# Performance work log

Measured on AMD Instinct MI355X. Metric: run time of the kernel, lower is better.

Reference implementation:

```python
import jax, jax.numpy as jnp
import numpy as np

GROUPS = 8
EPS = 1e-5


def setup_inputs() -> dict:
    key = jax.random.key(0)
    ks = jax.random.split(key, 3)
    b, c, h, w = 8, 256, 64, 64
    return {
        "x": jax.random.normal(ks[0], (b, c, h, w), dtype=jnp.float32),
        "norm_w": jnp.ones((c,), jnp.float32),
        "norm_b": jnp.zeros((c,), jnp.float32),
        "qkv_w": jax.random.normal(ks[1], (3 * c, c), dtype=jnp.float32) * (1.0 / np.sqrt(c)),
        "qkv_b": jnp.zeros((3 * c,), jnp.float32),
        "proj_w": jax.random.normal(ks[2], (c, c), dtype=jnp.float32) * (1.0 / np.sqrt(c)),
        "proj_b": jnp.zeros((c,), jnp.float32),
    }


def _group_norm(x, w, b):
    B, C, H, W = x.shape
    xg = x.reshape(B, GROUPS, C // GROUPS, H, W)
    mean = xg.mean(axis=(2, 3, 4), keepdims=True)
    var = xg.var(axis=(2, 3, 4), keepdims=True)
    xn = ((xg - mean) * jax.lax.rsqrt(var + EPS)).reshape(B, C, H, W)
    return xn * w[None, :, None, None] + b[None, :, None, None]


def reference(x, norm_w, norm_b, qkv_w, qkv_b, proj_w, proj_b):
    B, C, H, W = x.shape
    xn = _group_norm(x, norm_w, norm_b)
    # 1x1 conv == per-pixel matmul: [B,3C,H,W]
    qkv = jnp.einsum('bchw,oc->bohw', xn, qkv_w) + qkv_b[None, :, None, None]
    q, k, v = jnp.split(qkv, 3, axis=1)  # each [B,C,H,W]
    hw = H * W
    q = q.reshape(B, C, hw).transpose(0, 2, 1)  # [B,hw,C]
    k = k.reshape(B, C, hw)                     # [B,C,hw]
    v = v.reshape(B, C, hw).transpose(0, 2, 1)  # [B,hw,C]
    scores = jnp.einsum('bnc,bcm->bnm', q, k) / jnp.sqrt(jnp.asarray(C, x.dtype))
    attn = jax.nn.softmax(scores, axis=-1)      # [B,hw,hw]
    out = jnp.einsum('bnm,bmc->bnc', attn, v)   # [B,hw,C]
    out = out.transpose(0, 2, 1).reshape(B, C, H, W)
    out = jnp.einsum('bchw,oc->bohw', out, proj_w) + proj_b[None, :, None, None]
    return x + out
```

## Files before the change

kernel.cpp:

```cpp
#include <hip/hip_runtime.h>
#include <stdint.h>

#define BATCH 8
#define CH 256
#define HW 4096
#define OC 768

typedef __bf16 bf16;
typedef __attribute__((ext_vector_type(8))) __bf16 bf16x8;
typedef __attribute__((ext_vector_type(4))) __bf16 bf16x4;
typedef __attribute__((ext_vector_type(4))) float f32x4;
typedef __attribute__((ext_vector_type(4))) int i32x4;
typedef __attribute__((ext_vector_type(8))) int i32x8;
typedef long fp8x8;

#define MFMA16(a, b, c) __builtin_amdgcn_mfma_f32_16x16x32_bf16(a, b, c, 0, 0, 0)
#define MFMA8(a, b, c) __builtin_amdgcn_mfma_f32_16x16x32_fp8_fp8(a, b, c, 0, 0, 0)
#define MFMA_MX(a, b, c) __builtin_amdgcn_mfma_scale_f32_16x16x128_f8f6f4( \
    a, b, c, 0, 0, 0, 0x7F7F7F7F, 0, 0x7F7F7F7F)
#define LOG2E 1.44269504088896f

static __device__ __forceinline__ void gl2lds16(const void* g, void* l) {
  __builtin_amdgcn_global_load_lds((const __attribute__((address_space(1))) void*)g,
                                   (__attribute__((address_space(3))) void*)l, 16, 0, 0);
}

static __device__ __forceinline__ int pack4fp8(float a, float b, float c, float d) {
  int t = __builtin_amdgcn_cvt_pk_fp8_f32(a, b, 0, false);
  return __builtin_amdgcn_cvt_pk_fp8_f32(c, d, t, true);
}

__global__ __launch_bounds__(256) void trans_stats(const float* __restrict__ x,
    bf16* __restrict__ xt, float* __restrict__ partial) {
  __shared__ float tile[64][65];
  __shared__ float red[16];
  int b = blockIdx.z, ct = blockIdx.y, pt = blockIdx.x;
  int p0 = pt * 64, c0 = ct * 64;
  int tid = threadIdx.x;
  const float* xb = x + (size_t)b * CH * HW;
  float s[2] = {0.f, 0.f}, s2[2] = {0.f, 0.f};
#pragma unroll
  for (int i = 0; i < 4; i++) {
    int idx = i * 256 + tid;
    int c = idx >> 4, p4 = (idx & 15) * 4;
    float4 v = *(const float4*)(xb + (size_t)(c0 + c) * HW + p0 + p4);
    tile[c][p4] = v.x; tile[c][p4 + 1] = v.y; tile[c][p4 + 2] = v.z; tile[c][p4 + 3] = v.w;
    int g = i >> 1;
    s[g] += v.x + v.y + v.z + v.w;
    s2[g] += v.x * v.x + v.y * v.y + v.z * v.z + v.w * v.w;
  }
  for (int off = 32; off; off >>= 1) {
    s[0] += __shfl_down(s[0], off); s2[0] += __shfl_down(s2[0], off);
    s[1] += __shfl_down(s[1], off); s2[1] += __shfl_down(s2[1], off);
  }
  int wv = tid >> 6;
  if ((tid & 63) == 0) {
    red[wv * 4 + 0] = s[0]; red[wv * 4 + 1] = s2[0];
    red[wv * 4 + 2] = s[1]; red[wv * 4 + 3] = s2[1];
  }
  __syncthreads();
  if (tid < 2) {
    float ts = 0.f, ts2 = 0.f;
#pragma unroll
    for (int k = 0; k < 4; k++) { ts += red[k * 4 + tid * 2]; ts2 += red[k * 4 + tid * 2 + 1]; }
    float* pp = partial + ((size_t)(b * 8 + ct * 2 + tid) * 64 + pt) * 2;
    pp[0] = ts; pp[1] = ts2;
  }
  bf16* xtb = xt + (size_t)b * HW * CH;
#pragma unroll
  for (int i = 0; i < 2; i++) {
    int idx = i * 256 + tid;
    int p = idx >> 3, c8 = (idx & 7) * 8;
    bf16x8 v;
#pragma unroll
    for (int j = 0; j < 8; j++) v[j] = (bf16)tile[c8 + j][p];
    *(bf16x8*)(&xtb[(size_t)(p0 + p) * CH + c0 + c8]) = v;
  }
}

__global__ __launch_bounds__(64) void gn_finalize(const float* __restrict__ partial,
    const float* __restrict__ nw, const float* __restrict__ nb,
    float* __restrict__ scale, float* __restrict__ shift) {
  int bg = blockIdx.x;
  int t = threadIdx.x;
  const float* pp = partial + (size_t)bg * 64 * 2;
  float s = pp[t * 2], s2 = pp[t * 2 + 1];
  __shared__ float mm[2];
  for (int off = 32; off; off >>= 1) { s += __shfl_down(s, off); s2 += __shfl_down(s2, off); }
  if (t == 0) {
    float mean = s * (1.0f / 131072.0f);
    float var = s2 * (1.0f / 131072.0f) - mean * mean;
    mm[0] = mean;
    mm[1] = rsqrtf(var + 1e-5f);
  }
  __syncthreads();
  if (t < 32) {
    int b = bg >> 3, g = bg & 7, c = g * 32 + t;
    float sc = nw[c] * mm[1];
    scale[b * CH + c] = sc;
    shift[b * CH + c] = nb[c] - mm[0] * sc;
  }
}

__global__ __launch_bounds__(256) void fold_qkv(const float* __restrict__ qkv_w,
    const float* __restrict__ qkv_b, const float* __restrict__ scale,
    const float* __restrict__ shift, bf16* __restrict__ wq, float* __restrict__ bq) {
  int o = blockIdx.x, b = blockIdx.y, c = threadIdx.x;
  float w = qkv_w[o * CH + c];
  wq[((size_t)b * OC + o) * CH + c] = (bf16)(w * scale[b * CH + c]);
  float part = w * shift[b * CH + c];
  __shared__ float red[4];
  for (int off = 32; off; off >>= 1) part += __shfl_down(part, off);
  if ((threadIdx.x & 63) == 0) red[threadIdx.x >> 6] = part;
  __syncthreads();
  if (threadIdx.x == 0) bq[b * OC + o] = qkv_b[o] + red[0] + red[1] + red[2] + red[3];
}

__global__ __launch_bounds__(256) void conv_projw(const float* __restrict__ w,
                                                  bf16* __restrict__ wb) {
  int i = blockIdx.x * 256 + threadIdx.x;
  wb[i] = (bf16)w[i];
}

__global__ __launch_bounds__(256) void qkv_gemm(const bf16* __restrict__ wq,
    const float* __restrict__ bq, const bf16* __restrict__ xt,
    uint8_t* __restrict__ qt, uint8_t* __restrict__ kt, uint8_t* __restrict__ vv) {
  __shared__ __align__(16) bf16 As[2][128 * 32];
  __shared__ __align__(16) bf16 Bs[2][128 * 32];
  int b = blockIdx.z, row0 = blockIdx.y * 128, col0 = blockIdx.x * 128;
  const bf16* A = wq + (size_t)b * OC * CH + (size_t)row0 * CH;
  const bf16* Bt = xt + (size_t)b * HW * CH + (size_t)col0 * CH;
  int tid = threadIdx.x, lane = tid & 63, wave = tid >> 6;
  int wm = (wave & 1) * 64, wn = (wave >> 1) * 64;
  int l15 = lane & 15, quad = lane >> 4;
  auto stage = [&](int buf, int k0) {
#pragma unroll
    for (int i = 0; i < 2; i++) {
      int idx = i * 256 + tid, r = idx >> 2, ch = idx & 3;
      gl2lds16(A + (size_t)r * CH + k0 + ch * 8, &As[buf][idx * 8]);
    }
#pragma unroll
    for (int i = 0; i < 2; i++) {
      int idx = i * 256 + tid, r = idx >> 2, ch = idx & 3;
      gl2lds16(Bt + (size_t)r * CH + k0 + ch * 8, &Bs[buf][idx * 8]);
    }
  };
  f32x4 zero = {0.f, 0.f, 0.f, 0.f};
  f32x4 acc[4][4];
#pragma unroll
  for (int i = 0; i < 4; i++)
#pragma unroll
    for (int j = 0; j < 4; j++) acc[i][j] = zero;
  stage(0, 0);
  for (int kk = 0; kk < 8; kk++) {
    int cur = kk & 1;
    __syncthreads();
    if (kk < 7) stage(1 - cur, (kk + 1) * 32);
    bf16x8 af[4], bfr[4];
#pragma unroll
    for (int i = 0; i < 4; i++) {
      af[i] = *(const bf16x8*)(&As[cur][(wm + i * 16 + l15) * 32 + quad * 8]);
      bfr[i] = *(const bf16x8*)(&Bs[cur][(wn + i * 16 + l15) * 32 + quad * 8]);
    }
#pragma unroll
    for (int i = 0; i < 4; i++)
#pragma unroll
      for (int j = 0; j < 4; j++) acc[i][j] = MFMA16(af[i], bfr[j], acc[i][j]);
  }
  __syncthreads();
  uint8_t* tb = (uint8_t*)&As[0][0];
  int y = blockIdx.y;
  if (y < 4) {
    float sc = (y < 2) ? LOG2E : 1.0f;
#pragma unroll
    for (int i = 0; i < 4; i++) {
      int o_l = wm + i * 16 + quad * 4;
#pragma unroll
      for (int j = 0; j < 4; j++) {
        int p_l = wn + j * 16 + l15;
        float v[4];
#pragma unroll
        for (int r = 0; r < 4; r++) v[r] = (acc[i][j][r] + bq[b * OC + row0 + o_l + r]) * sc;
        *(int*)(tb + p_l * 128 + (o_l ^ ((p_l & 7) << 4))) =
            pack4fp8(v[0], v[1], v[2], v[3]);
      }
    }
    __syncthreads();
    uint8_t* dst = (y < 2) ? (qt + (size_t)b * HW * CH + row0)
                           : (kt + (size_t)b * HW * CH + (row0 - 256));
#pragma unroll
    for (int ii = 0; ii < 4; ii++) {
      int idx = ii * 256 + tid, p_l = idx >> 3, k = idx & 7;
      i32x4 d = *(const i32x4*)(tb + p_l * 128 + ((k * 16) ^ ((p_l & 7) << 4)));
      *(i32x4*)(dst + (size_t)(col0 + p_l) * CH + k * 16) = d;
    }
  } else {
#pragma unroll
    for (int i = 0; i < 4; i++) {
      int o_l = wm + i * 16 + quad * 4;
      int swz = ((o_l >> 2) & 7) << 4;
#pragma unroll
      for (int j = 0; j < 4; j++) {
        int p_l = wn + j * 16 + l15;
#pragma unroll
        for (int r = 0; r < 4; r++) {
          float vf = acc[i][j][r] + bq[b * OC + row0 + o_l + r];
          int t8 = __builtin_amdgcn_cvt_pk_fp8_f32(vf, 0.f, 0, false);
          tb[(o_l + r) * 128 + (p_l ^ swz)] = (uint8_t)(t8 & 0xff);
        }
      }
    }
    __syncthreads();
    uint8_t* dst = vv + ((size_t)b * CH + (row0 - 512)) * HW + col0;
#pragma unroll
    for (int ii = 0; ii < 4; ii++) {
      int idx = ii * 256 + tid, c_l = idx >> 3, k = idx & 7;
      i32x4 d = *(const i32x4*)(tb + c_l * 128 + ((k * 16) ^ (((c_l >> 2) & 7) << 4)));
      *(i32x4*)(dst + (size_t)c_l * HW + k * 16) = d;
    }
  }
}

__global__ __launch_bounds__(256, 2) void attn(const uint8_t* __restrict__ qt,
    const uint8_t* __restrict__ kt, const uint8_t* __restrict__ vv,
    bf16* __restrict__ opart, float* __restrict__ lstat) {
  __shared__ __align__(16) uint8_t Ks[2][32 * 256];
  __shared__ __align__(16) uint8_t Vs[3][256 * 32];
  int lin = blockIdx.x + 32 * (blockIdx.y + 2 * blockIdx.z);
  int pair = (lin & 7) * 2 + ((lin >> 3) & 1);
  int b = pair >> 1, mh = pair & 1, q0 = (lin >> 4) * 128;
  int tid = threadIdx.x, lane = tid & 63, w = tid >> 6;
  int l15 = lane & 15, quad = lane >> 4;
  int q1 = quad >> 1, qh = quad & 1;
  const uint8_t* kb_base = kt + (size_t)b * HW * CH;
  const uint8_t* vb_base = vv + (size_t)b * CH * HW;
  auto stageK = [&](int buf, int m0) {
    const uint8_t* kb = kb_base + (size_t)m0 * CH;
#pragma unroll
    for (int i = 0; i < 2; i++) {
      int idx = i * 256 + tid, m = idx >> 4, p16 = idx & 15;
      gl2lds16(kb + m * CH + (p16 ^ (m & 7)) * 16, &Ks[buf][idx * 16]);
    }
  };
  auto stageV = [&](int buf, int m0) {
#pragma unroll
    for (int i = 0; i < 2; i++) {
      int idx = i * 256 + tid, c = idx >> 1;
      int h2 = (idx & 1) ^ ((idx >> 3) & 1);
      gl2lds16(vb_base + (size_t)c * HW + m0 + h2 * 16, &Vs[buf][idx * 16]);
    }
  };
  i32x8 qf[2][2];
  const uint8_t* qb = qt + ((size_t)b * HW + q0 + w * 32) * CH;
#pragma unroll
  for (int ns = 0; ns < 2; ns++)
#pragma unroll
    for (int kc = 0; kc < 2; kc++) {
      const uint8_t* p = qb + (size_t)(ns * 16 + l15) * CH + kc * 128 + quad * 32;
      i32x4 lo = *(const i32x4*)p;
      i32x4 hi = *(const i32x4*)(p + 16);
      i32x8 q8 = {lo[0], lo[1], lo[2], lo[3], hi[0], hi[1], hi[2], hi[3]};
      qf[ns][kc] = q8;
    }
  f32x4 zero = {0.f, 0.f, 0.f, 0.f};
  f32x4 o[2][16];
#pragma unroll
  for (int ns = 0; ns < 2; ns++)
#pragma unroll
    for (int t = 0; t < 16; t++) o[ns][t] = zero;
  float lsum[2] = {0.f, 0.f};
  int kswz = l15 & 7;
  int vswz = (l15 >> 2) & 1;

  auto qk = [&](int kbuf, f32x4 (&s)[2][2]) {
#pragma unroll
    for (int kc = 0; kc < 2; kc++) {
#pragma unroll
      for (int ms = 0; ms < 2; ms++) {
        const uint8_t* base = &Ks[kbuf][(ms * 16 + l15) * 256];
        i32x4 lo = *(const i32x4*)(base + (((kc * 8 + quad * 2 + 0) ^ kswz) * 16));
        i32x4 hi = *(const i32x4*)(base + (((kc * 8 + quad * 2 + 1) ^ kswz) * 16));
        i32x8 kf = {lo[0], lo[1], lo[2], lo[3], hi[0], hi[1], hi[2], hi[3]};
#pragma unroll
        for (int ns = 0; ns < 2; ns++) s[ms][ns] = MFMA_MX(kf, qf[ns][kc], s[ms][ns]);
      }
    }
  };
  auto softmax = [&](f32x4 (&s)[2][2], fp8x8 (&paOut)[2]) {
#pragma unroll
    for (int ns = 0; ns < 2; ns++) {
      float p0[4], p1[4];
#pragma unroll
      for (int r = 0; r < 4; r++) {
        p0[r] = exp2f(fmaf(s[0][ns][r], 0.0625f, -2.0f));
        lsum[ns] += p0[r];
      }
#pragma unroll
      for (int r = 0; r < 4; r++) {
        p1[r] = exp2f(fmaf(s[1][ns][r], 0.0625f, -2.0f));
        lsum[ns] += p1[r];
      }
      int pk0 = pack4fp8(p0[0], p0[1], p0[2], p0[3]);
      int pk1 = pack4fp8(p1[0], p1[1], p1[2], p1[3]);
      int srcLo = ((quad & 1) * 32 + l15) << 2;
      int srcHi = srcLo + 64;
      int a0 = __builtin_amdgcn_ds_bpermute(srcLo, pk0);
      int a1 = __builtin_amdgcn_ds_bpermute(srcLo, pk1);
      int b0 = __builtin_amdgcn_ds_bpermute(srcHi, pk0);
      int b1 = __builtin_amdgcn_ds_bpermute(srcHi, pk1);
      int2 pr;
      pr.x = q1 ? a1 : a0;
      pr.y = q1 ? b1 : b0;
      paOut[ns] = __builtin_bit_cast(long, pr);
    }
  };
  auto pv_half = [&](int vbuf, fp8x8 (&pa)[2], int t0) {
#pragma unroll
    for (int t8 = 0; t8 < 8; t8++) {
      int t = t0 + t8;
      fp8x8 vf = *(const fp8x8*)(&Vs[vbuf][(2 * (t * 16 + l15) + (q1 ^ vswz)) * 16 + qh * 8]);
      o[0][t] = MFMA8(vf, pa[0], o[0][t]);
      o[1][t] = MFMA8(vf, pa[1], o[1][t]);
    }
  };

  int m0base = mh * 2048;
  int vread = 0;
  int vstage = 2;
  stageK(0, m0base);
  stageV(0, m0base);
  stageK(1, m0base + 32);
  stageV(1, m0base + 32);
  __syncthreads();
  fp8x8 paA[2], paB[2];
  {
    f32x4 s[2][2] = {{zero, zero}, {zero, zero}};
    qk(0, s);
    softmax(s, paA);
  }
  auto body = [&](int i, fp8x8 (&paPrev)[2], fp8x8 (&paCur)[2]) {
    int kcur = i & 1;
    __syncthreads();
    if (i < 63) {
      int m0n = m0base + (i + 1) * 32;
      stageK(1 - kcur, m0n);
      stageV(vstage, m0n);
      vstage = (vstage == 2) ? 0 : vstage + 1;
    }
    f32x4 s[2][2] = {{zero, zero}, {zero, zero}};
    __builtin_amdgcn_s_setprio(1);
    qk(kcur, s);
    pv_half(vread, paPrev, 0);
    softmax(s, paCur);
    pv_half(vread, paPrev, 8);
    __builtin_amdgcn_s_setprio(0);
    vread = (vread == 2) ? 0 : vread + 1;
  };
  for (int ii = 1; ii <= 61; ii += 2) {
    body(ii, paA, paB);
    body(ii + 1, paB, paA);
  }
  body(63, paA, paB);
  pv_half(vread, paB, 0);
  pv_half(vread, paB, 8);
  int ncol = q0 + w * 32 + l15;
  int pq = quad >> 1, par = quad & 1;
#pragma unroll
  for (int ns = 0; ns < 2; ns++) {
    float lt = lsum[ns];
    lt += __shfl_xor(lt, 16);
    lt += __shfl_xor(lt, 32);
    float inv = 1.0f / lt;
    bf16* ob = opart + ((size_t)(mh * BATCH + b) * HW + ncol + ns * 16) * CH;
#pragma unroll
    for (int t = 0; t < 16; t++) {
      bf16x4 pk;
#pragma unroll
      for (int r = 0; r < 4; r++) pk[r] = (bf16)(o[ns][t][r] * inv);
      int2 my = __builtin_bit_cast(int2, pk);
      int2 ex;
      ex.x = __shfl_xor(my.x, 16);
      ex.y = __shfl_xor(my.y, 16);
      if ((t & 1) == par) {
        i32x4 v;
        if (par == 0) { v[0] = my.x; v[1] = my.y; v[2] = ex.x; v[3] = ex.y; }
        else          { v[0] = ex.x; v[1] = ex.y; v[2] = my.x; v[3] = my.y; }
        *(i32x4*)(&ob[t * 16 + pq * 8]) = v;
      }
    }
    if (quad == 0)
      lstat[(size_t)(mh * BATCH + b) * HW + ncol + ns * 16] = lt;
  }
}

__global__ __launch_bounds__(256) void proj_gemm(const bf16* __restrict__ pw,
    const float* __restrict__ pbias, const bf16* __restrict__ opart,
    const float* __restrict__ lstat, const float* __restrict__ x,
    float* __restrict__ out) {
  __shared__ __align__(16) bf16 As[2][128 * 32];
  __shared__ __align__(16) bf16 Bs[2][128 * 32];
  int b = blockIdx.z, row0 = blockIdx.y * 128, col0 = blockIdx.x * 128;
  const bf16* A = pw + (size_t)row0 * CH;
  const bf16* op0 = opart + ((size_t)(0 * BATCH + b) * HW + col0) * CH;
  const bf16* op1 = opart + ((size_t)(1 * BATCH + b) * HW + col0) * CH;
  int tid = threadIdx.x, lane = tid & 63, wave = tid >> 6;
  int wm = (wave & 1) * 64, wn = (wave >> 1) * 64;
  int l15 = lane & 15, quad = lane >> 4;
  float w0a[2], w1a[2];
#pragma unroll
  for (int i = 0; i < 2; i++) {
    int p = col0 + i * 64 + (tid >> 2);
    float l0 = lstat[(size_t)(0 * BATCH + b) * HW + p];
    float l1 = lstat[(size_t)(1 * BATCH + b) * HW + p];
    float inv = 1.0f / (l0 + l1);
    w0a[i] = l0 * inv;
    w1a[i] = l1 * inv;
  }
  auto stageA = [&](int buf, int k0) {
#pragma unroll
    for (int i = 0; i < 2; i++) {
      int idx = i * 256 + tid, r = idx >> 2, ch = idx & 3;
      gl2lds16(A + (size_t)r * CH + k0 + ch * 8, &As[buf][idx * 8]);
    }
  };
  auto loadB = [&](int k0, bf16x8 (&b0)[2], bf16x8 (&b1)[2]) {
#pragma unroll
    for (int i = 0; i < 2; i++) {
      int r = i * 64 + (tid >> 2), ch = tid & 3;
      b0[i] = *(const bf16x8*)(op0 + (size_t)r * CH + k0 + ch * 8);
      b1[i] = *(const bf16x8*)(op1 + (size_t)r * CH + k0 + ch * 8);
    }
  };
  auto writeB = [&](int buf, bf16x8 (&b0)[2], bf16x8 (&b1)[2]) {
#pragma unroll
    for (int i = 0; i < 2; i++) {
      int idx = i * 256 + tid;
      bf16x8 o8;
#pragma unroll
      for (int j = 0; j < 8; j++)
        o8[j] = (bf16)(w0a[i] * (float)b0[i][j] + w1a[i] * (float)b1[i][j]);
      *(bf16x8*)(&Bs[buf][idx * 8]) = o8;
    }
  };
  f32x4 zero = {0.f, 0.f, 0.f, 0.f};
  f32x4 acc[4][4];
#pragma unroll
  for (int i = 0; i < 4; i++)
#pragma unroll
    for (int j = 0; j < 4; j++) acc[i][j] = zero;
  bf16x8 nb0[2], nb1[2];
  stageA(0, 0);
  loadB(0, nb0, nb1);
  writeB(0, nb0, nb1);
  for (int kk = 0; kk < 8; kk++) {
    int cur = kk & 1;
    __syncthreads();
    if (kk < 7) {
      stageA(1 - cur, (kk + 1) * 32);
      loadB((kk + 1) * 32, nb0, nb1);
    }
    bf16x8 af[4], bfr[4];
#pragma unroll
    for (int i = 0; i < 4; i++) {
      af[i] = *(const bf16x8*)(&As[cur][(wm + i * 16 + l15) * 32 + quad * 8]);
      bfr[i] = *(const bf16x8*)(&Bs[cur][(wn + i * 16 + l15) * 32 + quad * 8]);
    }
#pragma unroll
    for (int i = 0; i < 4; i++)
#pragma unroll
      for (int j = 0; j < 4; j++) acc[i][j] = MFMA16(af[i], bfr[j], acc[i][j]);
    if (kk < 7) writeB(1 - cur, nb0, nb1);
  }
#pragma unroll
  for (int i = 0; i < 4; i++) {
#pragma unroll
    for (int j = 0; j < 4; j++) {
      int p = col0 + wn + j * 16 + l15;
#pragma unroll
      for (int r = 0; r < 4; r++) {
        int oo = row0 + wm + i * 16 + quad * 4 + r;
        size_t off = ((size_t)b * CH + oo) * HW + p;
        out[off] = x[off] + pbias[oo] + acc[i][j][r];
      }
    }
  }
}

extern "C" void kernel_launch(void* const* d_in, const int* in_sizes, int n_in,
                              void* d_out, int out_size, void* d_ws, size_t ws_size,
                              hipStream_t stream) {
  const float* x = (const float*)d_in[0];
  const float* nw = (const float*)d_in[1];
  const float* nb = (const float*)d_in[2];
  const float* qkvw = (const float*)d_in[3];
  const float* qkvb = (const float*)d_in[4];
  const float* projw = (const float*)d_in[5];
  const float* projb = (const float*)d_in[6];
  float* out = (float*)d_out;
  char* ws = (char*)d_ws;
  float* scale = (float*)(ws + 0);
  float* shift = (float*)(ws + 8192);
  float* bq    = (float*)(ws + 16384);
  bf16* pwb    = (bf16*)(ws + 40960);
  bf16* wq     = (bf16*)(ws + 172032);
  bf16* xt     = (bf16*)(ws + 3317760);
  uint8_t* qt  = (uint8_t*)(ws + 20094976);
  uint8_t* kt  = (uint8_t*)(ws + 36872192);
  uint8_t* vv  = (uint8_t*)(ws + 53649408);
  bf16* opart  = (bf16*)(ws + 70426624);
  float* lstat = (float*)(ws + 103981056);
  float* partial = (float*)(ws + 70426624);

  trans_stats<<<dim3(64, 4, 8), 256, 0, stream>>>(x, xt, partial);
  gn_finalize<<<64, 64, 0, stream>>>(partial, nw, nb, scale, shift);
  fold_qkv<<<dim3(768, 8), 256, 0, stream>>>(qkvw, qkvb, scale, shift, wq, bq);
  conv_projw<<<256, 256, 0, stream>>>(projw, pwb);
  qkv_gemm<<<dim3(32, 6, 8), 256, 0, stream>>>(wq, bq, xt, qt, kt, vv);
  attn<<<dim3(32, 2, 8), 256, 0, stream>>>(qt, kt, vv, opart, lstat);
  proj_gemm<<<dim3(32, 2, 8), 256, 0, stream>>>(pwb, projb, opart, lstat, x, out);
}
```

Before: 257.8 us.

## Vectorize fold_qkv, drop conv_projw launch, remap GEMM grids batch-fastest

fold_qkv now has each wave handle one output row with float4 loads and a shuffle-only reduction, so the shared-memory reduction and block barrier go away. The separate projection-weight bf16 conversion kernel is removed; proj_gemm instead loads fp32 weights into registers and converts them to bf16 as it writes LDS. Both GEMMs use a linearized 1D grid with batch as the fastest index, which changes the order in which tiles are scheduled and how the L2 cache is reused. The trade-off is that the register-staged A path in proj_gemm replaces the async global-to-LDS copy and reads twice the bytes per weight element.

```diff
diff --git a/kernel.cpp b/kernel.cpp
--- a/kernel.cpp
+++ b/kernel.cpp
@@ -105,21 +105,22 @@
 __global__ __launch_bounds__(256) void fold_qkv(const float* __restrict__ qkv_w,
     const float* __restrict__ qkv_b, const float* __restrict__ scale,
     const float* __restrict__ shift, bf16* __restrict__ wq, float* __restrict__ bq) {
-  int o = blockIdx.x, b = blockIdx.y, c = threadIdx.x;
-  float w = qkv_w[o * CH + c];
-  wq[((size_t)b * OC + o) * CH + c] = (bf16)(w * scale[b * CH + c]);
-  float part = w * shift[b * CH + c];
-  __shared__ float red[4];
+  int b = blockIdx.y;
+  int o = blockIdx.x * 4 + (threadIdx.x >> 6);
+  int lane = threadIdx.x & 63;
+  int c = lane * 4;
+  float4 w = *(const float4*)(qkv_w + (size_t)o * CH + c);
+  float4 sc = *(const float4*)(scale + b * CH + c);
+  float4 sh = *(const float4*)(shift + b * CH + c);
+  bf16x4 wo;
+  wo[0] = (bf16)(w.x * sc.x);
+  wo[1] = (bf16)(w.y * sc.y);
+  wo[2] = (bf16)(w.z * sc.z);
+  wo[3] = (bf16)(w.w * sc.w);
+  *(bf16x4*)(wq + ((size_t)b * OC + o) * CH + c) = wo;
+  float part = w.x * sh.x + w.y * sh.y + w.z * sh.z + w.w * sh.w;
   for (int off = 32; off; off >>= 1) part += __shfl_down(part, off);
-  if ((threadIdx.x & 63) == 0) red[threadIdx.x >> 6] = part;
-  __syncthreads();
-  if (threadIdx.x == 0) bq[b * OC + o] = qkv_b[o] + red[0] + red[1] + red[2] + red[3];
-}
-
-__global__ __launch_bounds__(256) void conv_projw(const float* __restrict__ w,
-                                                  bf16* __restrict__ wb) {
-  int i = blockIdx.x * 256 + threadIdx.x;
-  wb[i] = (bf16)w[i];
+  if (lane == 0) bq[b * OC + o] = qkv_b[o] + part;
 }
 
 __global__ __launch_bounds__(256) void qkv_gemm(const bf16* __restrict__ wq,
@@ -127,7 +128,11 @@
     uint8_t* __restrict__ qt, uint8_t* __restrict__ kt, uint8_t* __restrict__ vv) {
   __shared__ __align__(16) bf16 As[2][128 * 32];
   __shared__ __align__(16) bf16 Bs[2][128 * 32];
-  int b = blockIdx.z, row0 = blockIdx.y * 128, col0 = blockIdx.x * 128;
+  int lin = blockIdx.x;
+  int b = lin & 7;
+  int rest = lin >> 3;
+  int y = rest % 6, colt = rest / 6;
+  int row0 = y * 128, col0 = colt * 128;
   const bf16* A = wq + (size_t)b * OC * CH + (size_t)row0 * CH;
   const bf16* Bt = xt + (size_t)b * HW * CH + (size_t)col0 * CH;
   int tid = threadIdx.x, lane = tid & 63, wave = tid >> 6;
@@ -169,7 +174,6 @@
   }
   __syncthreads();
   uint8_t* tb = (uint8_t*)&As[0][0];
-  int y = blockIdx.y;
   if (y < 4) {
     float sc = (y < 2) ? LOG2E : 1.0f;
 #pragma unroll
@@ -393,14 +397,17 @@
   }
 }
 
-__global__ __launch_bounds__(256) void proj_gemm(const bf16* __restrict__ pw,
+__global__ __launch_bounds__(256) void proj_gemm(const float* __restrict__ pw,
     const float* __restrict__ pbias, const bf16* __restrict__ opart,
     const float* __restrict__ lstat, const float* __restrict__ x,
     float* __restrict__ out) {
   __shared__ __align__(16) bf16 As[2][128 * 32];
   __shared__ __align__(16) bf16 Bs[2][128 * 32];
-  int b = blockIdx.z, row0 = blockIdx.y * 128, col0 = blockIdx.x * 128;
-  const bf16* A = pw + (size_t)row0 * CH;
+  int lin = blockIdx.x;
+  int b = lin & 7;
+  int rest = lin >> 3;
+  int row0 = (rest & 1) * 128, col0 = (rest >> 1) * 128;
+  const float* A = pw + (size_t)row0 * CH;
   const bf16* op0 = opart + ((size_t)(0 * BATCH + b) * HW + col0) * CH;
   const bf16* op1 = opart + ((size_t)(1 * BATCH + b) * HW + col0) * CH;
   int tid = threadIdx.x, lane = tid & 63, wave = tid >> 6;
@@ -416,11 +423,25 @@
     w0a[i] = l0 * inv;
     w1a[i] = l1 * inv;
   }
-  auto stageA = [&](int buf, int k0) {
+  auto loadA = [&](int k0, float4 (&a4)[2][2]) {
 #pragma unroll
     for (int i = 0; i < 2; i++) {
       int idx = i * 256 + tid, r = idx >> 2, ch = idx & 3;
-      gl2lds16(A + (size_t)r * CH + k0 + ch * 8, &As[buf][idx * 8]);
+      const float* src = A + (size_t)r * CH + k0 + ch * 8;
+      a4[i][0] = *(const float4*)src;
+      a4[i][1] = *(const float4*)(src + 4);
+    }
+  };
+  auto writeA = [&](int buf, float4 (&a4)[2][2]) {
+#pragma unroll
+    for (int i = 0; i < 2; i++) {
+      int idx = i * 256 + tid;
+      bf16x8 o8;
+      o8[0] = (bf16)a4[i][0].x; o8[1] = (bf16)a4[i][0].y;
+      o8[2] = (bf16)a4[i][0].z; o8[3] = (bf16)a4[i][0].w;
+      o8[4] = (bf16)a4[i][1].x; o8[5] = (bf16)a4[i][1].y;
+      o8[6] = (bf16)a4[i][1].z; o8[7] = (bf16)a4[i][1].w;
+      *(bf16x8*)(&As[buf][idx * 8]) = o8;
     }
   };
   auto loadB = [&](int k0, bf16x8 (&b0)[2], bf16x8 (&b1)[2]) {
@@ -448,15 +469,17 @@
   for (int i = 0; i < 4; i++)
 #pragma unroll
     for (int j = 0; j < 4; j++) acc[i][j] = zero;
+  float4 a4[2][2];
   bf16x8 nb0[2], nb1[2];
-  stageA(0, 0);
+  loadA(0, a4);
   loadB(0, nb0, nb1);
+  writeA(0, a4);
   writeB(0, nb0, nb1);
   for (int kk = 0; kk < 8; kk++) {
     int cur = kk & 1;
     __syncthreads();
     if (kk < 7) {
-      stageA(1 - cur, (kk + 1) * 32);
+      loadA((kk + 1) * 32, a4);
       loadB((kk + 1) * 32, nb0, nb1);
     }
     bf16x8 af[4], bfr[4];
@@ -469,7 +492,10 @@
     for (int i = 0; i < 4; i++)
 #pragma unroll
       for (int j = 0; j < 4; j++) acc[i][j] = MFMA16(af[i], bfr[j], acc[i][j]);
-    if (kk < 7) writeB(1 - cur, nb0, nb1);
+    if (kk < 7) {
+      writeA(1 - cur, a4);
+      writeB(1 - cur, nb0, nb1);
+    }
   }
 #pragma unroll
   for (int i = 0; i < 4; i++) {
@@ -501,7 +527,6 @@
   float* scale = (float*)(ws + 0);
   float* shift = (float*)(ws + 8192);
   float* bq    = (float*)(ws + 16384);
-  bf16* pwb    = (bf16*)(ws + 40960);
   bf16* wq     = (bf16*)(ws + 172032);
   bf16* xt     = (bf16*)(ws + 3317760);
   uint8_t* qt  = (uint8_t*)(ws + 20094976);
@@ -513,9 +538,8 @@
 
   trans_stats<<<dim3(64, 4, 8), 256, 0, stream>>>(x, xt, partial);
   gn_finalize<<<64, 64, 0, stream>>>(partial, nw, nb, scale, shift);
-  fold_qkv<<<dim3(768, 8), 256, 0, stream>>>(qkvw, qkvb, scale, shift, wq, bq);
-  conv_projw<<<256, 256, 0, stream>>>(projw, pwb);
-  qkv_gemm<<<dim3(32, 6, 8), 256, 0, stream>>>(wq, bq, xt, qt, kt, vv);
+  fold_qkv<<<dim3(192, 8), 256, 0, stream>>>(qkvw, qkvb, scale, shift, wq, bq);
+  qkv_gemm<<<1536, 256, 0, stream>>>(wq, bq, xt, qt, kt, vv);
   attn<<<dim3(32, 2, 8), 256, 0, stream>>>(qt, kt, vv, opart, lstat);
-  proj_gemm<<<dim3(32, 2, 8), 256, 0, stream>>>(pwb, projb, opart, lstat, x, out);
-}
+  proj_gemm<<<512, 256, 0, stream>>>(projw, projb, opart, lstat, x, out);
+}
```

After: 253.6 us. Within noise of the previous version (-1.6%).
